# Kernel optimization log

Hardware: AMD Instinct MI355X
Metric: run time of the kernel (lower is better)

The kernel has to match this reference:

```python
import jax, jax.numpy as jnp
import numpy as np

B, S, D = 4, 2048, 16
N_HEAD_ARG = 16
# Faithful to source bug: effective num heads = hidden_size (D), head_size = D // n_head_arg.
# This only type-checks when head_size == 1 (D == n_head_arg), as in the repo config.
HEADS = D                     # self.n_head = hidden_size
HEAD_SIZE = D // N_HEAD_ARG   # = 1


def setup_inputs() -> dict:
    key = jax.random.key(0)
    k_x, k_wq, k_bq, k_wo, k_bo = jax.random.split(key, 5)
    x = jax.random.normal(k_x, (B, S, D), dtype=jnp.float32)
    # torch Linear init scale ~ 1/sqrt(in_features); store weights as [in, out]
    s = 1.0 / np.sqrt(D)
    w_qkv = jax.random.uniform(k_wq, (D, 3 * D), minval=-s, maxval=s, dtype=jnp.float32)
    b_qkv = jax.random.uniform(k_bq, (3 * D,), minval=-s, maxval=s, dtype=jnp.float32)
    w_out = jax.random.uniform(k_wo, (D, D), minval=-s, maxval=s, dtype=jnp.float32)
    b_out = jax.random.uniform(k_bo, (D,), minval=-s, maxval=s, dtype=jnp.float32)
    return {"x": x, "w_qkv": w_qkv, "b_qkv": b_qkv, "w_out": w_out, "b_out": b_out}


def reference(x, w_qkv, b_qkv, w_out, b_out):
    b, s, _ = x.shape
    qkv = x @ w_qkv + b_qkv                      # [b, s, 3D]
    q, k, v = jnp.split(qkv, 3, axis=-1)         # each [b, s, D]
    # [b, s, H, hs] -> [b, H, s, hs]
    q = q.reshape(b, s, HEADS, HEAD_SIZE).transpose(0, 2, 1, 3)
    k = k.reshape(b, s, HEADS, HEAD_SIZE).transpose(0, 2, 1, 3)
    v = v.reshape(b, s, HEADS, HEAD_SIZE).transpose(0, 2, 1, 3)
    scale = 1.0 / jnp.sqrt(jnp.asarray(HEAD_SIZE, dtype=x.dtype))
    scores = jnp.einsum('bhqd,bhkd->bhqk', q, k) * scale   # [b, H, s, s]
    causal = jnp.tril(jnp.ones((s, s), dtype=bool))
    scores = jnp.where(causal, scores, jnp.asarray(-jnp.inf, dtype=scores.dtype))
    attn = jax.nn.softmax(scores, axis=-1)
    # dropout is identity in eval mode (correctness baseline)
    out = jnp.einsum('bhqk,bhkd->bhqd', attn, v)            # [b, H, s, hs]
    out = out.transpose(0, 2, 1, 3).reshape(b, s, HEADS * HEAD_SIZE)
    return out @ w_out + b_out
```

## Files before the change

### kernel.cpp

```cpp
#include <hip/hip_runtime.h>
#include <math.h>

#define BB 4
#define SS 2048
#define DD 16
#define HH 16
#define NM 32

#define EXP2(x) __builtin_amdgcn_exp2f(x)
#define LOG2E 1.44269504088896340736f

__constant__ float INVFACT[NM] = {
    1.000000000e+00f, 1.000000000e+00f, 5.000000000e-01f, 1.666666667e-01f,
    4.166666667e-02f, 8.333333333e-03f, 1.388888889e-03f, 1.984126984e-04f,
    2.480158730e-05f, 2.755731922e-06f, 2.755731922e-07f, 2.505210839e-08f,
    2.087675699e-09f, 1.605904384e-10f, 1.147074560e-11f, 7.647163732e-13f,
    4.779477332e-14f, 2.811457254e-15f, 1.561920697e-16f, 8.220635247e-18f,
    4.110317623e-19f, 1.957294106e-20f, 8.896791392e-22f, 3.868170171e-23f,
    1.611737571e-24f, 6.446950284e-26f, 2.479596263e-27f, 9.183689864e-29f,
    3.279889237e-30f, 1.130996289e-31f, 3.769987629e-33f, 1.216125042e-34f};

#define UNPACK16(X4, XR)                                                   \
  const float4 x0_ = (X4)[0], x1_ = (X4)[1], x2_ = (X4)[2], x3_ = (X4)[3]; \
  const float XR[16] = {x0_.x, x0_.y, x0_.z, x0_.w, x1_.x, x1_.y, x1_.z,   \
                        x1_.w, x2_.x, x2_.y, x2_.z, x2_.w, x3_.x, x3_.y,   \
                        x3_.z, x3_.w};

__global__ __launch_bounds__(1024) void fused_attn_kernel(
    const float* __restrict__ x, const float* __restrict__ w_qkv,
    const float* __restrict__ b_qkv, float* __restrict__ AO) {
  __shared__ float kl[SS];
  __shared__ float vl[SS];
  __shared__ float ql[SS];
  __shared__ float2 SP[32 * 32];

  const int bh = blockIdx.x;
  const int b = bh >> 4, h = bh & 15;
  const int t = threadIdx.x;

  {
    float wq[16], wk[16], wv[16];
#pragma unroll
    for (int i = 0; i < 16; ++i) {
      wq[i] = w_qkv[i * 48 + h];
      wk[i] = w_qkv[i * 48 + 16 + h];
      wv[i] = w_qkv[i * 48 + 32 + h];
    }
    const float bq = b_qkv[h], bk = b_qkv[16 + h], bv = b_qkv[32 + h];
#pragma unroll
    for (int rr = 0; rr < 2; ++rr) {
      const int j = rr * 1024 + t;
      const float4* X4 = (const float4*)(x + ((size_t)b * SS + j) * DD);
      UNPACK16(X4, xr);
      float qq = bq, kk = bk, vv = bv;
#pragma unroll
      for (int i = 0; i < 16; ++i) {
        qq = fmaf(xr[i], wq[i], qq);
        kk = fmaf(xr[i], wk[i], kk);
        vv = fmaf(xr[i], wv[i], vv);
      }
      ql[j] = qq;
      kl[j] = kk;
      vl[j] = vv;
    }
  }
  __syncthreads();

  {
    const int m = t & 31;
    const int jb = t >> 5;
    const float c = INVFACT[m];
    float s = 0.f, tv = 0.f;
    const int base = jb * 64;
    for (int u = 0; u < 64; ++u) {
      const float k = kl[base + u];
      const float v = vl[base + u];
      const float k2 = k * k, k4 = k2 * k2, k8 = k4 * k4, k16 = k8 * k8;
      float p = (m & 1) ? k : 1.f;
      p *= (m & 2) ? k2 : 1.f;
      p *= (m & 4) ? k4 : 1.f;
      p *= (m & 8) ? k8 : 1.f;
      p *= (m & 16) ? k16 : 1.f;
      s += p;
      tv = fmaf(p, v, tv);
    }
    SP[t] = make_float2(s * c, tv * c);
  }
  __syncthreads();

  {
    const int jb = t >> 5;
#pragma unroll
    for (int off = 1; off < 32; off <<= 1) {
      const float2 self = SP[t];
      float2 othr = make_float2(0.f, 0.f);
      if (jb >= off) othr = SP[t - off * 32];
      __syncthreads();
      SP[t] = make_float2(self.x + othr.x, self.y + othr.y);
      __syncthreads();
    }
  }

  for (int rr = 0; rr < 2; ++rr) {
    const int i = rr * 1024 + t;
    const int lane = i & 63;
    const int qb = i >> 6;
    const float q = ql[i];
    const float qs = q * LOG2E;

    float num = 0.f, den = 0.f;
    if (qb > 0) {
      const float2* bc2 = SP + (size_t)(qb - 1) * 32;
      float p = 1.f;
#pragma unroll
      for (int m = 0; m < NM; ++m) {
        const float2 st = bc2[m];
        den = fmaf(p, st.x, den);
        num = fmaf(p, st.y, num);
        p *= q;
      }
    }

    float ld = 0.f, ad = 0.f;
    const float4* kd4 = (const float4*)(kl + qb * 64);
    const float4* vd4 = (const float4*)(vl + qb * 64);
#pragma unroll
    for (int g = 0; g < 16; ++g) {
      const float4 k4 = kd4[g], v4 = vd4[g];
      const int jj = 4 * g;
      float e;
      e = EXP2(qs * k4.x); e = (jj + 0 <= lane) ? e : 0.f; ld += e; ad = fmaf(e, v4.x, ad);
      e = EXP2(qs * k4.y); e = (jj + 1 <= lane) ? e : 0.f; ld += e; ad = fmaf(e, v4.y, ad);
      e = EXP2(qs * k4.z); e = (jj + 2 <= lane) ? e : 0.f; ld += e; ad = fmaf(e, v4.z, ad);
      e = EXP2(qs * k4.w); e = (jj + 3 <= lane) ? e : 0.f; ld += e; ad = fmaf(e, v4.w, ad);
    }

    AO[(size_t)bh * SS + i] = (ad + num) / (ld + den);
  }
}

__global__ __launch_bounds__(256) void proj_kernel(
    const float* __restrict__ AO, const float* __restrict__ w,
    const float* __restrict__ bias, float* __restrict__ out) {
  __shared__ float wct[DD * 68];
  __shared__ float aol[256];
  __shared__ float bs[DD];
  const int t = threadIdx.x;
  const int b = blockIdx.x >> 7;
  const int s_base = (blockIdx.x * 16) & (SS - 1);

  wct[(t & 15) * 68 + (t >> 4)] = w[t];
  if (t < DD) bs[t] = bias[t];
  {
    const int h = t >> 4, row_l = t & 15;
    const int bh = b * HH + h;
    aol[row_l * 16 + h] = AO[(size_t)bh * SS + s_base + row_l];
  }
  __syncthreads();

  const int row_l = t >> 4, d = t & 15;
  const float4* ao4 = (const float4*)aol;
  const float4* wc4 = (const float4*)wct;

  float y = bs[d];
#pragma unroll
  for (int g = 0; g < 4; ++g) {
    const float4 xv = ao4[row_l * 4 + g];
    const float4 wv = wc4[d * 17 + g];
    y = fmaf(xv.x, wv.x, y);
    y = fmaf(xv.y, wv.y, y);
    y = fmaf(xv.z, wv.z, y);
    y = fmaf(xv.w, wv.w, y);
  }
  out[(size_t)blockIdx.x * 256 + t] = y;
}

extern "C" void kernel_launch(void* const* d_in, const int* in_sizes, int n_in,
                              void* d_out, int out_size, void* d_ws,
                              size_t ws_size, hipStream_t stream) {
  const float* x = (const float*)d_in[0];
  const float* w_qkv = (const float*)d_in[1];
  const float* b_qkv = (const float*)d_in[2];
  const float* w_out = (const float*)d_in[3];
  const float* b_out = (const float*)d_in[4];
  float* out = (float*)d_out;

  float* AO = (float*)d_ws;

  fused_attn_kernel<<<64, 1024, 0, stream>>>(x, w_qkv, b_qkv, AO);
  proj_kernel<<<512, 256, 0, stream>>>(AO, w_out, b_out, out);
}
```

Before: 77.61 us.

## Split each head's queries across four blocks and serialize the prefix scan

Each (batch, head) is now handled by four blocks, each owning a 512-query slice. A block only computes K/V up to the end of its slice and Q only for its own slice, so the work is causally trimmed. The log-step shared-memory prefix scan with many barriers is replaced by a sequential scan done by 64 threads. The aim is to fill more CUs (256 blocks instead of 64), at the cost of recomputing K/V and the moment sums redundantly across blocks and leaving half the threads idle in the final phase.

```diff
diff --git a/kernel.cpp b/kernel.cpp
--- a/kernel.cpp
+++ b/kernel.cpp
@@ -31,12 +31,17 @@
     const float* __restrict__ b_qkv, float* __restrict__ AO) {
   __shared__ float kl[SS];
   __shared__ float vl[SS];
-  __shared__ float ql[SS];
+  __shared__ float ql[512];
   __shared__ float2 SP[32 * 32];
 
-  const int bh = blockIdx.x;
+  const int blk = blockIdx.x;
+  const int sub = blk & 3;
+  const int bh = blk >> 2;
   const int b = bh >> 4, h = bh & 15;
   const int t = threadIdx.x;
+  const int R = (sub + 1) * 512;
+  const int NB = (sub + 1) * 8;
+  const int q0 = sub * 512;
 
   {
     float wq[16], wk[16], wv[16];
@@ -47,21 +52,26 @@
       wv[i] = w_qkv[i * 48 + 32 + h];
     }
     const float bq = b_qkv[h], bk = b_qkv[16 + h], bv = b_qkv[32 + h];
-#pragma unroll
-    for (int rr = 0; rr < 2; ++rr) {
-      const int j = rr * 1024 + t;
-      const float4* X4 = (const float4*)(x + ((size_t)b * SS + j) * DD);
-      UNPACK16(X4, xr);
-      float qq = bq, kk = bk, vv = bv;
-#pragma unroll
-      for (int i = 0; i < 16; ++i) {
-        qq = fmaf(xr[i], wq[i], qq);
-        kk = fmaf(xr[i], wk[i], kk);
-        vv = fmaf(xr[i], wv[i], vv);
+    for (int r = 0; r * 1024 < R; ++r) {
+      const int j = r * 1024 + t;
+      if (j < R) {
+        const float4* X4 = (const float4*)(x + ((size_t)b * SS + j) * DD);
+        UNPACK16(X4, xr);
+        float kk = bk, vv = bv;
+#pragma unroll
+        for (int i = 0; i < 16; ++i) {
+          kk = fmaf(xr[i], wk[i], kk);
+          vv = fmaf(xr[i], wv[i], vv);
+        }
+        kl[j] = kk;
+        vl[j] = vv;
+        if ((unsigned)(j - q0) < 512u) {
+          float qq = bq;
+#pragma unroll
+          for (int i = 0; i < 16; ++i) qq = fmaf(xr[i], wq[i], qq);
+          ql[j - q0] = qq;
+        }
       }
-      ql[j] = qq;
-      kl[j] = kk;
-      vl[j] = vv;
     }
   }
   __syncthreads();
@@ -69,43 +79,43 @@
   {
     const int m = t & 31;
     const int jb = t >> 5;
-    const float c = INVFACT[m];
-    float s = 0.f, tv = 0.f;
-    const int base = jb * 64;
-    for (int u = 0; u < 64; ++u) {
-      const float k = kl[base + u];
-      const float v = vl[base + u];
-      const float k2 = k * k, k4 = k2 * k2, k8 = k4 * k4, k16 = k8 * k8;
-      float p = (m & 1) ? k : 1.f;
-      p *= (m & 2) ? k2 : 1.f;
-      p *= (m & 4) ? k4 : 1.f;
-      p *= (m & 8) ? k8 : 1.f;
-      p *= (m & 16) ? k16 : 1.f;
-      s += p;
-      tv = fmaf(p, v, tv);
-    }
-    SP[t] = make_float2(s * c, tv * c);
-  }
-  __syncthreads();
-
-  {
-    const int jb = t >> 5;
-#pragma unroll
-    for (int off = 1; off < 32; off <<= 1) {
-      const float2 self = SP[t];
-      float2 othr = make_float2(0.f, 0.f);
-      if (jb >= off) othr = SP[t - off * 32];
-      __syncthreads();
-      SP[t] = make_float2(self.x + othr.x, self.y + othr.y);
-      __syncthreads();
-    }
-  }
-
-  for (int rr = 0; rr < 2; ++rr) {
-    const int i = rr * 1024 + t;
+    if (jb < NB) {
+      const float c = INVFACT[m];
+      float s = 0.f, tv = 0.f;
+      const int base = jb * 64;
+      for (int u = 0; u < 64; ++u) {
+        const float k = kl[base + u];
+        const float v = vl[base + u];
+        const float k2 = k * k, k4 = k2 * k2, k8 = k4 * k4, k16 = k8 * k8;
+        float p = (m & 1) ? k : 1.f;
+        p *= (m & 2) ? k2 : 1.f;
+        p *= (m & 4) ? k4 : 1.f;
+        p *= (m & 8) ? k8 : 1.f;
+        p *= (m & 16) ? k16 : 1.f;
+        s += p;
+        tv = fmaf(p, v, tv);
+      }
+      SP[t] = make_float2(s * c, tv * c);
+    }
+  }
+  __syncthreads();
+
+  if (t < 64) {
+    float* SPf = (float*)SP;
+    const int off = ((t & 31) << 1) | (t >> 5);
+    float run = 0.f;
+    for (int jb = 0; jb < NB; ++jb) {
+      run += SPf[jb * 64 + off];
+      SPf[jb * 64 + off] = run;
+    }
+  }
+  __syncthreads();
+
+  if (t < 512) {
+    const int i = q0 + t;
     const int lane = i & 63;
     const int qb = i >> 6;
-    const float q = ql[i];
+    const float q = ql[t];
     const float qs = q * LOG2E;
 
     float num = 0.f, den = 0.f;
@@ -187,6 +197,6 @@
 
   float* AO = (float*)d_ws;
 
-  fused_attn_kernel<<<64, 1024, 0, stream>>>(x, w_qkv, b_qkv, AO);
+  fused_attn_kernel<<<256, 1024, 0, stream>>>(x, w_qkv, b_qkv, AO);
   proj_kernel<<<512, 256, 0, stream>>>(AO, w_out, b_out, out);
 }
```

Result: faster. 73.40 us (-5.4%).
